# Kernel optimization log

Measured on AMD Instinct MI355X. Metric: run time of the kernel, lower is better.

The kernel has to match this reference:

```python
import jax, jax.numpy as jnp
import numpy as np
import math

B, T, D = 32, 1024, 512
K, H = 64, 4
KP = K // H
MLP = 4 * D


def setup_inputs() -> dict:
    key = jax.random.key(0)
    ks = jax.random.split(key, 8)
    return {
        "x": jax.random.normal(ks[0], (B, T, D), jnp.float32),
        "w_in": jax.random.normal(ks[1], (D, 2 * K), jnp.float32) / math.sqrt(D),
        "log_decay": jax.random.uniform(ks[2], (K,), jnp.float32, -3.0, -0.1),
        "frequency": jnp.linspace(0.0, 2.0 * math.pi * (1.0 - 1.0 / K), K, dtype=jnp.float32),
        "coupling": jnp.broadcast_to(jnp.eye(KP, dtype=jnp.float32), (H, KP, KP))
                    + 0.01 * jax.random.normal(ks[3], (H, KP, KP), jnp.float32) / math.sqrt(KP),
        "w_out": jax.random.normal(ks[4], (2 * K, D), jnp.float32) / math.sqrt(2 * K),
        "w_gate": jax.random.normal(ks[5], (D, D), jnp.float32) / math.sqrt(D),
        "b_gate": jnp.full((D,), -2.0, jnp.float32),
        "w1": jax.random.normal(ks[6], (D, MLP), jnp.float32) / math.sqrt(D),
        "b1": jnp.zeros((MLP,), jnp.float32),
        "w2": jax.random.normal(ks[7], (MLP, D), jnp.float32) / math.sqrt(MLP),
        "b2": jnp.zeros((D,), jnp.float32),
        "g1": jnp.ones((D,), jnp.float32),
        "bn1": jnp.zeros((D,), jnp.float32),
        "g2": jnp.ones((D,), jnp.float32),
        "bn2": jnp.zeros((D,), jnp.float32),
    }


def _ln(x, g, b):
    m = jnp.mean(x, axis=-1, keepdims=True)
    v = jnp.var(x, axis=-1, keepdims=True)
    return (x - m) * jax.lax.rsqrt(v + 1e-5) * g + b


def reference(x, w_in, log_decay, frequency, coupling, w_out, w_gate, b_gate,
              w1, b1, w2, b2, g1, bn1, g2, bn2):
    Bv, Tv, Dv = x.shape
    residual = x
    xn = _ln(x, g1, bn1)
    beta = xn @ w_in                                   # [B,T,2K]
    beta_r, beta_i = jnp.split(beta, 2, axis=-1)       # each [B,T,K]
    # eigenstate kernel: lambda_k^n = sigmoid(log_decay)^n * exp(i n freq)
    mag = jax.nn.sigmoid(log_decay)                    # [K]
    n = jnp.arange(Tv, dtype=x.dtype)
    mag_pow = mag[None, :] ** n[:, None]               # [T,K]
    phase = n[:, None] * frequency[None, :]            # [T,K]
    kernel = jax.lax.complex(mag_pow * jnp.cos(phase), mag_pow * jnp.sin(phase))
    beta_c = jax.lax.complex(beta_r, beta_i)           # [B,T,K] complex
    # zero-pad to 2T for linear (causal) convolution via FFT
    B_f = jnp.fft.fft(jnp.pad(beta_c, ((0, 0), (0, Tv), (0, 0))), axis=1)  # [B,2T,K]
    K_f = jnp.fft.fft(jnp.pad(kernel, ((0, Tv), (0, 0))), axis=0)          # [2T,K]
    c = jnp.fft.ifft(B_f * K_f[None], axis=1)[:, :Tv, :]                   # [B,T,K]
    c_r, c_i = jnp.real(c), jnp.imag(c)
    # per-head coupling: block-diagonal matmul over eigenstates
    nh, kp = coupling.shape[0], coupling.shape[1]
    c_rh = c_r.reshape(Bv, Tv, nh, kp)
    c_ih = c_i.reshape(Bv, Tv, nh, kp)
    c_r = jnp.einsum('hjk,bthk->bthj', coupling, c_rh).reshape(Bv, Tv, nh * kp)
    c_i = jnp.einsum('hjk,bthk->bthj', coupling, c_ih).reshape(Bv, Tv, nh * kp)
    eigenstates = jnp.concatenate([c_r, c_i], axis=-1)  # [B,T,2K]
    h = eigenstates @ w_out                             # [B,T,D]
    gate = jax.nn.sigmoid(xn @ w_gate + b_gate)
    x1 = residual + gate * h
    xn2 = _ln(x1, g2, bn2)
    mlp = jax.nn.silu(xn2 @ w1 + b1) @ w2 + b2
    out = x1 + mlp
    return out, eigenstates
```

## Files before the change

kernel.cpp:

```cpp
#include <hip/hip_runtime.h>
#include <math.h>
#include <stdint.h>

#define Bb   32
#define Tt   1024
#define Dd   512
#define Kk   64
#define K2   128
#define Hh   4
#define KP   16
#define MLPD 2048
#define Mrows (Bb * Tt)

#define CW 48
#define CT 64

typedef unsigned short ushort_t;
typedef __attribute__((ext_vector_type(8))) short short8;
typedef __attribute__((ext_vector_type(4))) float floatx4;

__device__ __forceinline__ float sigf(float x) { return 1.0f / (1.0f + __expf(-x)); }

__device__ __forceinline__ ushort_t f2bf(float f) {
    unsigned u = __float_as_uint(f);
    u += 0x7fffu + ((u >> 16) & 1u);
    return (ushort_t)(u >> 16);
}
__device__ __forceinline__ float bf2f(ushort_t h) {
    return __uint_as_float(((unsigned)h) << 16);
}

__device__ __forceinline__ void async16(const void* g, void* l) {
    __builtin_amdgcn_global_load_lds((const __attribute__((address_space(1))) void*)g,
                                     (__attribute__((address_space(3))) void*)l, 16, 0, 0);
}

__global__ __launch_bounds__(256) void ln_bf_kernel(const float* __restrict__ x,
                                                    const float* __restrict__ g,
                                                    const float* __restrict__ b,
                                                    ushort_t* __restrict__ o) {
    int row  = blockIdx.x * 4 + (threadIdx.x >> 6);
    int lane = threadIdx.x & 63;
    const float4* xr = (const float4*)(x + (size_t)row * Dd);
    float4 a = xr[lane];
    float4 c = xr[lane + 64];
    float s = a.x + a.y + a.z + a.w + c.x + c.y + c.z + c.w;
    float q = a.x * a.x + a.y * a.y + a.z * a.z + a.w * a.w
            + c.x * c.x + c.y * c.y + c.z * c.z + c.w * c.w;
#pragma unroll
    for (int m = 32; m > 0; m >>= 1) {
        s += __shfl_xor(s, m);
        q += __shfl_xor(q, m);
    }
    float mean = s * (1.0f / Dd);
    float var  = q * (1.0f / Dd) - mean * mean;
    float rs   = rsqrtf(var + 1e-5f);
    const float4* gg = (const float4*)g;
    const float4* bb = (const float4*)b;
    float4 g0 = gg[lane], g1 = gg[lane + 64];
    float4 b0 = bb[lane], b1 = bb[lane + 64];
    ushort4 r0, r1;
    r0.x = f2bf((a.x - mean) * rs * g0.x + b0.x);
    r0.y = f2bf((a.y - mean) * rs * g0.y + b0.y);
    r0.z = f2bf((a.z - mean) * rs * g0.z + b0.z);
    r0.w = f2bf((a.w - mean) * rs * g0.w + b0.w);
    r1.x = f2bf((c.x - mean) * rs * g1.x + b1.x);
    r1.y = f2bf((c.y - mean) * rs * g1.y + b1.y);
    r1.z = f2bf((c.z - mean) * rs * g1.z + b1.z);
    r1.w = f2bf((c.w - mean) * rs * g1.w + b1.w);
    ushort4* oo = (ushort4*)(o + (size_t)row * Dd);
    oo[lane]      = r0;
    oo[lane + 64] = r1;
}

__global__ __launch_bounds__(256) void convert_transpose(const float* __restrict__ in,
                                                         ushort_t* __restrict__ out,
                                                         int R, int C) {
    __shared__ float t[32][33];
    int bx = blockIdx.x * 32;
    int by = blockIdx.y * 32;
    int tc = threadIdx.x & 31, tr = threadIdx.x >> 5;
#pragma unroll
    for (int i = 0; i < 4; i++)
        t[tr + 8 * i][tc] = in[(size_t)(by + tr + 8 * i) * C + bx + tc];
    __syncthreads();
#pragma unroll
    for (int i = 0; i < 4; i++)
        out[(size_t)(bx + tr + 8 * i) * R + by + tc] = f2bf(t[tc][tr + 8 * i]);
}

__global__ void kern_precompute(const float* __restrict__ log_decay,
                                const float* __restrict__ freq,
                                float* __restrict__ kern) {
    int i = blockIdx.x * 256 + threadIdx.x;
    if (i >= CW * Kk) return;
    int d = i >> 6, k = i & 63;
    float mag = 1.0f / (1.0f + expf(-log_decay[k]));
    float mp  = powf(mag, (float)d);
    float ph  = (float)d * freq[k];
    kern[d * K2 + k]      = mp * cosf(ph);
    kern[d * K2 + 64 + k] = mp * sinf(ph);
}

__global__ __launch_bounds__(256) void conv_kernel(const float* __restrict__ beta,
                                                   const float* __restrict__ kern,
                                                   const float* __restrict__ coup,
                                                   float* __restrict__ eig,
                                                   ushort_t* __restrict__ eigb) {
    __shared__ float sBeta[CT + CW][K2];
    __shared__ float sCoup[Hh][KP][KP];
    int b   = blockIdx.y;
    int t0  = blockIdx.x * CT;
    int tid = threadIdx.x;
    for (int i = tid; i < Hh * KP * KP; i += 256) {
        int h = i >> 8, j = (i >> 4) & 15, kk = i & 15;
        sCoup[h][kk][j] = coup[i];
    }
    for (int i = tid; i < (CT + CW) * K2; i += 256) {
        int r = i >> 7, c = i & 127;
        int t = t0 - CW + r;
        sBeta[r][c] = (t >= 0) ? beta[((size_t)b * Tt + t) * K2 + c] : 0.0f;
    }
    __syncthreads();
    int k  = tid & 63;
    int ts = tid >> 6;
    float cr[16], ci[16];
#pragma unroll
    for (int i = 0; i < 16; i++) { cr[i] = 0.0f; ci[i] = 0.0f; }
    for (int d = 0; d < CW; d++) {
        float kr = kern[d * K2 + k];
        float ki = kern[d * K2 + 64 + k];
#pragma unroll
        for (int i = 0; i < 16; i++) {
            int r    = CW + ts + 4 * i - d;
            float br = sBeta[r][k];
            float bi = sBeta[r][64 + k];
            cr[i] += kr * br - ki * bi;
            ci[i] += kr * bi + ki * br;
        }
    }
    __syncthreads();
#pragma unroll
    for (int i = 0; i < 16; i++) {
        int tl = ts + 4 * i;
        sBeta[tl][k]      = cr[i];
        sBeta[tl][64 + k] = ci[i];
    }
    __syncthreads();
    int h = k >> 4, jj = k & 15;
#pragma unroll
    for (int i = 0; i < 16; i++) {
        int tl = ts + 4 * i;
        float er = 0.0f, ei = 0.0f;
#pragma unroll
        for (int kk = 0; kk < KP; kk++) {
            float w = sCoup[h][kk][jj];
            er += w * sBeta[tl][h * KP + kk];
            ei += w * sBeta[tl][64 + h * KP + kk];
        }
        size_t off = ((size_t)b * Tt + t0 + tl) * K2;
        eig[off + k]       = er;
        eig[off + 64 + k]  = ei;
        eigb[off + k]      = f2bf(er);
        eigb[off + 64 + k] = f2bf(ei);
    }
}

enum { EPI_INCOMB = 0, EPI_X1, EPI_SILU, EPI_OUT0, EPI_OUTA };

#define STG 16384

template <int EPI>
__global__ __launch_bounds__(256) void mfma_gemm(
    const ushort_t* __restrict__ A, const ushort_t* __restrict__ Bt,
    void* __restrict__ Cv, void* __restrict__ Cv2, int K, int ldb, int ldc,
    int gx,
    const float* __restrict__ bias,
    const float* __restrict__ aux1, const ushort_t* __restrict__ aux2) {
    __shared__ __align__(16) char lds[2 * STG];
    int tid  = threadIdx.x;
    int lane = tid & 63, w = tid >> 6;
    int lin  = blockIdx.x;
    int xcd  = lin & 7;
    int rest = lin >> 3;
    int bx   = rest % gx;
    int by   = xcd + 8 * (rest / gx);
    int bm = by * 128, bn = bx * 128;
    int wm = (w >> 1) * 64, wn = (w & 1) * 64;

    const char* gA[2];
    const char* gB[2];
    int lofsA[2], lofsB[2];
#pragma unroll
    for (int q = 0; q < 2; q++) {
        int c = 2 * w + q;
        int m = c * 16 + (lane >> 2);
        int g = ((lane & 3) - ((m >> 1) & 3)) & 3;
        gA[q] = (const char*)(A  + (size_t)(bm + m) * K   + g * 8);
        gB[q] = (const char*)(Bt + (size_t)(bn + m) * ldb + g * 8);
        lofsA[q] = c * 1024;
        lofsB[q] = 8192 + c * 1024;
    }
    int aoff[4], boff[4];
#pragma unroll
    for (int i = 0; i < 4; i++) {
        int m = wm + i * 16 + (lane & 15);
        aoff[i] = m * 64 + ((((lane >> 4) + (m >> 1)) & 3) * 16);
        int n = wn + i * 16 + (lane & 15);
        boff[i] = 8192 + n * 64 + ((((lane >> 4) + (n >> 1)) & 3) * 16);
    }
    floatx4 acc[4][4];
#pragma unroll
    for (int i = 0; i < 4; i++)
#pragma unroll
        for (int j = 0; j < 4; j++) acc[i][j] = (floatx4)0.0f;

    async16(gA[0], lds + lofsA[0]);
    async16(gA[1], lds + lofsA[1]);
    async16(gB[0], lds + lofsB[0]);
    async16(gB[1], lds + lofsB[1]);
    __syncthreads();

    int p = 0;
    for (int k0 = 0; k0 < K; k0 += 32) {
        if (k0 + 32 < K) {
            size_t kb = (size_t)(k0 + 32) * 2;
            char* d = lds + (p ^ 1) * STG;
            async16(gA[0] + kb, d + lofsA[0]);
            async16(gA[1] + kb, d + lofsA[1]);
            async16(gB[0] + kb, d + lofsB[0]);
            async16(gB[1] + kb, d + lofsB[1]);
        }
        const char* s = lds + p * STG;
        short8 af[4], bfr[4];
#pragma unroll
        for (int i = 0; i < 4; i++) af[i]  = *(const short8*)(s + aoff[i]);
#pragma unroll
        for (int j = 0; j < 4; j++) bfr[j] = *(const short8*)(s + boff[j]);
#pragma unroll
        for (int i = 0; i < 4; i++)
#pragma unroll
            for (int j = 0; j < 4; j++)
                acc[i][j] = __builtin_amdgcn_mfma_f32_16x16x32_bf16(af[i], bfr[j], acc[i][j], 0, 0, 0);
        __syncthreads();
        p ^= 1;
    }
    int rq = (lane >> 4) * 4;
    int cn = lane & 15;
#pragma unroll
    for (int i = 0; i < 4; i++) {
#pragma unroll
        for (int j = 0; j < 4; j++) {
            int col = bn + wn + j * 16 + cn;
#pragma unroll
            for (int r = 0; r < 4; r++) {
                int row    = bm + wm + i * 16 + rq + r;
                float v    = acc[i][j][r];
                if (EPI == EPI_INCOMB) {
                    if (bx == 0) {
                        ((float*)Cv)[(size_t)row * K2 + col] = v;
                    } else {
                        int gc = col - 128;
                        ((ushort_t*)Cv2)[(size_t)row * Dd + gc] = f2bf(sigf(v + bias[gc]));
                    }
                } else if (EPI == EPI_X1) {
                    size_t off = (size_t)row * ldc + col;
                    ((float*)Cv)[off] = aux1[off] + bf2f(aux2[off]) * v;
                } else if (EPI == EPI_SILU) {
                    size_t off = (size_t)row * ldc + col;
                    float t = v + bias[col];
                    ((ushort_t*)Cv)[off] = f2bf(t * sigf(t));
                } else if (EPI == EPI_OUT0) {
                    size_t off = (size_t)row * ldc + col;
                    float* C = (float*)Cv;
                    C[off] = C[off] + v + bias[col];
                } else {
                    size_t off = (size_t)row * ldc + col;
                    ((float*)Cv)[off] += v;
                }
            }
        }
    }
}

extern "C" void kernel_launch(void* const* d_in, const int* in_sizes, int n_in,
                              void* d_out, int out_size, void* d_ws, size_t ws_size,
                              hipStream_t stream) {
    (void)in_sizes; (void)n_in; (void)out_size;
    const float* x         = (const float*)d_in[0];
    const float* w_in      = (const float*)d_in[1];
    const float* log_decay = (const float*)d_in[2];
    const float* frequency = (const float*)d_in[3];
    const float* coupling  = (const float*)d_in[4];
    const float* w_out     = (const float*)d_in[5];
    const float* w_gate    = (const float*)d_in[6];
    const float* b_gate    = (const float*)d_in[7];
    const float* w1        = (const float*)d_in[8];
    const float* b1        = (const float*)d_in[9];
    const float* w2        = (const float*)d_in[10];
    const float* b2        = (const float*)d_in[11];
    const float* g1        = (const float*)d_in[12];
    const float* bn1       = (const float*)d_in[13];
    const float* g2        = (const float*)d_in[14];
    const float* bn2       = (const float*)d_in[15];

    float* out = (float*)d_out;
    float* eig = (float*)d_out + (size_t)Mrows * Dd;

    char* ws = (char*)d_ws;
    ushort_t* xn      = (ushort_t*)(ws);
    ushort_t* xn2     = (ushort_t*)(ws + (32ull  << 20));
    float*    beta    = (float*)   (ws + (64ull  << 20));
    ushort_t* eigb    = (ushort_t*)(ws + (80ull  << 20));
    ushort_t* gateb   = (ushort_t*)(ws + (88ull  << 20));
    ushort_t* w_comb  = (ushort_t*)(ws + (120ull << 20));
    ushort_t* w_outT  = (ushort_t*)(ws + (122ull << 20));
    ushort_t* w1T     = (ushort_t*)(ws + (123ull << 20));
    ushort_t* w2T     = (ushort_t*)(ws + (125ull << 20));
    float*    kern    = (float*)   (ws + (127ull << 20));

    size_t base = 128ull << 20;
    ushort_t* hid;
    int CC;
    if (ws_size >= base + ((size_t)Mrows * 2048 * 2)) { hid = (ushort_t*)(ws + base); CC = 2048; }
    else if (ws_size >= base + ((size_t)Mrows * 1024 * 2)) { hid = (ushort_t*)(ws + base); CC = 1024; }
    else { hid = (ushort_t*)ws; CC = 512; }
    int nch = MLPD / CC;

    dim3 blk(256);
    convert_transpose<<<dim3(K2 / 32, Dd / 32), blk, 0, stream>>>(w_in, w_comb, Dd, K2);
    convert_transpose<<<dim3(Dd / 32, Dd / 32), blk, 0, stream>>>(w_gate, w_comb + (size_t)K2 * Dd, Dd, Dd);
    convert_transpose<<<dim3(Dd / 32, K2 / 32), blk, 0, stream>>>(w_out, w_outT, K2, Dd);
    convert_transpose<<<dim3(MLPD / 32, Dd / 32), blk, 0, stream>>>(w1, w1T, Dd, MLPD);
    convert_transpose<<<dim3(Dd / 32, MLPD / 32), blk, 0, stream>>>(w2, w2T, MLPD, Dd);
    kern_precompute<<<dim3((CW * Kk + 255) / 256), blk, 0, stream>>>(log_decay, frequency, kern);

    ln_bf_kernel<<<dim3(Mrows / 4), blk, 0, stream>>>(x, g1, bn1, xn);
    mfma_gemm<EPI_INCOMB><<<dim3(5 * 256), blk, 0, stream>>>(
        xn, w_comb, beta, gateb, Dd, Dd, 0, 5, b_gate, nullptr, nullptr);
    conv_kernel<<<dim3(Tt / CT, Bb), blk, 0, stream>>>(beta, kern, coupling, eig, eigb);
    mfma_gemm<EPI_X1><<<dim3(4 * 256), blk, 0, stream>>>(
        eigb, w_outT, out, nullptr, K2, K2, Dd, 4, nullptr, x, gateb);
    ln_bf_kernel<<<dim3(Mrows / 4), blk, 0, stream>>>(out, g2, bn2, xn2);
    for (int c = 0; c < nch; c++) {
        mfma_gemm<EPI_SILU><<<dim3((CC / 128) * 256), blk, 0, stream>>>(
            xn2, w1T + (size_t)c * CC * Dd, hid, nullptr, Dd, Dd, CC, CC / 128, b1 + (size_t)c * CC, nullptr, nullptr);
        if (c == 0) {
            mfma_gemm<EPI_OUT0><<<dim3(4 * 256), blk, 0, stream>>>(
                hid, w2T + (size_t)c * CC, out, nullptr, CC, MLPD, Dd, 4, b2, nullptr, nullptr);
        } else {
            mfma_gemm<EPI_OUTA><<<dim3(4 * 256), blk, 0, stream>>>(
                hid, w2T + (size_t)c * CC, out, nullptr, CC, MLPD, Dd, 4, nullptr, nullptr, nullptr);
        }
    }
}
```

Measured before the change: 569.9 us.

## Replace async global-to-LDS loads with register-staged double buffering in GEMM

The GEMM main loop no longer uses the global_load_lds async copy. Each tile is now loaded into registers, written to an alternating LDS stage, and the next tile's global loads are issued before the barrier and the MFMA work. This removes the trailing barrier per iteration and lets global loads overlap compute through registers. In exchange it uses more VGPRs and adds explicit LDS store instructions. With only one barrier per step, the LDS stores of the next iteration could race with readers of the same stage from two iterations earlier, although double buffering keeps that safe.

```diff
diff --git a/kernel.cpp b/kernel.cpp
--- a/kernel.cpp
+++ b/kernel.cpp
@@ -28,11 +28,6 @@
 }
 __device__ __forceinline__ float bf2f(ushort_t h) {
     return __uint_as_float(((unsigned)h) << 16);
-}
-
-__device__ __forceinline__ void async16(const void* g, void* l) {
-    __builtin_amdgcn_global_load_lds((const __attribute__((address_space(1))) void*)g,
-                                     (__attribute__((address_space(3))) void*)l, 16, 0, 0);
 }
 
 __global__ __launch_bounds__(256) void ln_bf_kernel(const float* __restrict__ x,
@@ -198,8 +193,8 @@
         int g = ((lane & 3) - ((m >> 1) & 3)) & 3;
         gA[q] = (const char*)(A  + (size_t)(bm + m) * K   + g * 8);
         gB[q] = (const char*)(Bt + (size_t)(bn + m) * ldb + g * 8);
-        lofsA[q] = c * 1024;
-        lofsB[q] = 8192 + c * 1024;
+        lofsA[q] = c * 1024 + lane * 16;
+        lofsB[q] = 8192 + c * 1024 + lane * 16;
     }
     int aoff[4], boff[4];
 #pragma unroll
@@ -215,23 +210,27 @@
 #pragma unroll
         for (int j = 0; j < 4; j++) acc[i][j] = (floatx4)0.0f;
 
-    async16(gA[0], lds + lofsA[0]);
-    async16(gA[1], lds + lofsA[1]);
-    async16(gB[0], lds + lofsB[0]);
-    async16(gB[1], lds + lofsB[1]);
-    __syncthreads();
-
-    int p = 0;
-    for (int k0 = 0; k0 < K; k0 += 32) {
-        if (k0 + 32 < K) {
-            size_t kb = (size_t)(k0 + 32) * 2;
-            char* d = lds + (p ^ 1) * STG;
-            async16(gA[0] + kb, d + lofsA[0]);
-            async16(gA[1] + kb, d + lofsA[1]);
-            async16(gB[0] + kb, d + lofsB[0]);
-            async16(gB[1] + kb, d + lofsB[1]);
-        }
-        const char* s = lds + p * STG;
+    float4 rA0 = *(const float4*)gA[0];
+    float4 rA1 = *(const float4*)gA[1];
+    float4 rB0 = *(const float4*)gB[0];
+    float4 rB1 = *(const float4*)gB[1];
+
+    int ns = K >> 5;
+    for (int k = 0; k < ns; k++) {
+        char* st = lds + (size_t)(k & 1) * STG;
+        *(float4*)(st + lofsA[0]) = rA0;
+        *(float4*)(st + lofsA[1]) = rA1;
+        *(float4*)(st + lofsB[0]) = rB0;
+        *(float4*)(st + lofsB[1]) = rB1;
+        if (k + 1 < ns) {
+            size_t kb = (size_t)(k + 1) * 64;
+            rA0 = *(const float4*)(gA[0] + kb);
+            rA1 = *(const float4*)(gA[1] + kb);
+            rB0 = *(const float4*)(gB[0] + kb);
+            rB1 = *(const float4*)(gB[1] + kb);
+        }
+        __syncthreads();
+        const char* s = st;
         short8 af[4], bfr[4];
 #pragma unroll
         for (int i = 0; i < 4; i++) af[i]  = *(const short8*)(s + aoff[i]);
@@ -242,8 +241,6 @@
 #pragma unroll
             for (int j = 0; j < 4; j++)
                 acc[i][j] = __builtin_amdgcn_mfma_f32_16x16x32_bf16(af[i], bfr[j], acc[i][j], 0, 0, 0);
-        __syncthreads();
-        p ^= 1;
     }
     int rq = (lane >> 4) * 4;
     int cn = lane & 15;
```

Result: no change. 574.2 us (+0.8%).
